# Optimization experiments

Measured on AMD Instinct MI355X. Metric: run time of the kernel, lower is better.

Reference implementation:

```python
import jax, jax.numpy as jnp
import numpy as np

B, T, H, L = 8, 256, 64, 3
NB, NF, HP = 17, 68, 6
K = 9  # temporal kernel
PAD = (K - 1) // 2
EPS = 1e-5


def _normalize(adj):
    adj = adj + np.eye(adj.shape[0], dtype=np.float32)
    d = adj.sum(1)
    dinv = np.power(d, -0.5)
    dinv[np.isinf(dinv)] = 0.0
    return (dinv[:, None] * adj * dinv[None, :]).astype(np.float32)


def _body_adj():
    a = np.zeros((NB, NB), np.float32)
    conns = [(0, 1), (0, 2), (1, 3), (2, 4), (0, 5), (0, 6), (5, 6), (5, 7), (7, 9), (6, 8), (8, 10), (5, 11), (6, 12), (11, 12), (11, 13), (13, 15), (12, 14), (14, 16)]
    for i, j in conns:
        a[i, j] = 1.0
        a[j, i] = 1.0
    return _normalize(a)


def _face_adj():
    a = np.zeros((NF, NF), np.float32)
    for i in range(16): a[i, i + 1] = 1.0
    for i in range(17, 21): a[i, i + 1] = 1.0
    for i in range(22, 26): a[i, i + 1] = 1.0
    for i in range(27, 30): a[i, i + 1] = 1.0
    for i in range(31, 35): a[i, i + 1] = 1.0
    for i in range(36, 41): a[i, i + 1] = 1.0
    a[41, 36] = 1.0
    for i in range(42, 47): a[i, i + 1] = 1.0
    a[47, 42] = 1.0
    for i in range(48, 59): a[i, i + 1] = 1.0
    a[59, 48] = 1.0
    for i in range(60, 67): a[i, i + 1] = 1.0
    a[67, 60] = 1.0
    a = a + a.T
    return _normalize(a)


def setup_inputs() -> dict:
    keys = iter(jax.random.split(jax.random.key(0), 80))

    def rn(shape, s):
        return jax.random.normal(next(keys), shape, jnp.float32) * s

    inp = {}
    inp['body_kps'] = jax.random.normal(next(keys), (B, T, NB * 2), jnp.float32)
    inp['face_kps_2d'] = jax.random.normal(next(keys), (B, T, NF * 2), jnp.float32)
    inp['head_pose'] = jax.random.normal(next(keys), (B, T, HP), jnp.float32)
    inp['body_adj'] = jnp.asarray(_body_adj())
    inp['face_adj'] = jnp.asarray(_face_adj())
    inp['body_proj_w'] = rn((2, H), 0.5)
    inp['body_proj_b'] = jnp.zeros((H,), jnp.float32)
    inp['face_proj_w'] = rn((2, H), 0.5)
    inp['face_proj_b'] = jnp.zeros((H,), jnp.float32)
    inp['head_w'] = rn((HP, H), 0.3)
    inp['head_b'] = jnp.zeros((H,), jnp.float32)
    for p in ('b', 'f'):
        inp[p + '_t1w'] = rn((L, H, H, K), 0.04)
        inp[p + '_t1b'] = jnp.zeros((L, H), jnp.float32)
        inp[p + '_bn1g'] = jnp.ones((L, H), jnp.float32)
        inp[p + '_bn1b'] = jnp.zeros((L, H), jnp.float32)
        inp[p + '_bn1m'] = rn((L, H), 0.1)
        inp[p + '_bn1v'] = jax.random.uniform(next(keys), (L, H), jnp.float32, 0.5, 1.5)
        inp[p + '_gcw'] = rn((L, H, H), 0.1)
        inp[p + '_gcb'] = jnp.zeros((L, H), jnp.float32)
        inp[p + '_t2w'] = rn((L, H, H, K), 0.04)
        inp[p + '_t2b'] = jnp.zeros((L, H), jnp.float32)
        inp[p + '_bn2g'] = jnp.ones((L, H), jnp.float32)
        inp[p + '_bn2b'] = jnp.zeros((L, H), jnp.float32)
        inp[p + '_bn2m'] = rn((L, H), 0.1)
        inp[p + '_bn2v'] = jax.random.uniform(next(keys), (L, H), jnp.float32, 0.5, 1.5)
    total = NB * H + NF * H + H  # 5504
    inp['fus1_w'] = rn((total, 4 * H), 0.02)
    inp['fus1_b'] = jnp.zeros((4 * H,), jnp.float32)
    inp['fus2_w'] = rn((4 * H, 2 * H), 0.06)
    inp['fus2_b'] = jnp.zeros((2 * H,), jnp.float32)
    inp['fus3_w'] = rn((2 * H, H), 0.09)
    inp['fus3_b'] = jnp.zeros((H,), jnp.float32)
    inp['fus4_w'] = rn((H, 5), 0.12)
    inp['fus4_b'] = jnp.zeros((5,), jnp.float32)
    return inp


def _conv_bn(x, w, b, g, be, m, v):
    # x: (BN, C, T); w: (O, I, K). Conv1d (pad=4) + eval-mode BatchNorm1d.
    y = jax.lax.conv_general_dilated(x, w, (1,), [(PAD, PAD)], dimension_numbers=('NCH', 'OIH', 'NCH'))
    y = y + b[None, :, None]
    inv = g * jax.lax.rsqrt(v + EPS)
    return y * inv[None, :, None] + (be - m * inv)[None, :, None]


def _block(x, adj, t1w, t1b, g1, b1, m1, v1, gw, gb, t2w, t2b, g2, b2, m2, v2):
    # x: (B, N, C, T); residual is identity (in_channels == out_channels)
    Bn, N, C, Tn = x.shape
    res = x
    h = jax.nn.relu(_conv_bn(x.reshape(Bn * N, C, Tn), t1w, t1b, g1, b1, m1, v1)).reshape(Bn, N, C, Tn)
    # spatial graph conv, batched over all timesteps at once (adj @ (x W) + b)
    support = jnp.einsum('bnct,co->bnot', h, gw)
    h = jax.nn.relu(jnp.einsum('mn,bnot->bmot', adj, support) + gb[None, None, :, None])
    h = _conv_bn(h.reshape(Bn * N, C, Tn), t2w, t2b, g2, b2, m2, v2).reshape(Bn, N, C, Tn)
    return h + res  # dropout = identity in eval


def _stream(x, n_nodes, pw, pb, adj, ps):
    Bn, Tn, _ = x.shape
    h = x.reshape(Bn, Tn, n_nodes, 2) @ pw + pb          # (B, T, N, H)
    h = jnp.transpose(h, (0, 2, 3, 1))                   # (B, N, H, T)
    for l in range(ps[0].shape[0]):
        h = _block(h, adj, *(p[l] for p in ps))
    return h.mean(axis=3).reshape(Bn, -1)                # temporal mean-pool, flatten nodes


def reference(body_kps, face_kps_2d, head_pose, body_adj, face_adj, body_proj_w, body_proj_b, face_proj_w, face_proj_b, head_w, head_b, b_t1w, b_t1b, b_bn1g, b_bn1b, b_bn1m, b_bn1v, b_gcw, b_gcb, b_t2w, b_t2b, b_bn2g, b_bn2b, b_bn2m, b_bn2v, f_t1w, f_t1b, f_bn1g, f_bn1b, f_bn1m, f_bn1v, f_gcw, f_gcb, f_t2w, f_t2b, f_bn2g, f_bn2b, f_bn2m, f_bn2v, fus1_w, fus1_b, fus2_w, fus2_b, fus3_w, fus3_b, fus4_w, fus4_b):
    bps = (b_t1w, b_t1b, b_bn1g, b_bn1b, b_bn1m, b_bn1v, b_gcw, b_gcb, b_t2w, b_t2b, b_bn2g, b_bn2b, b_bn2m, b_bn2v)
    fps = (f_t1w, f_t1b, f_bn1g, f_bn1b, f_bn1m, f_bn1v, f_gcw, f_gcb, f_t2w, f_t2b, f_bn2g, f_bn2b, f_bn2m, f_bn2v)
    bf = _stream(body_kps, NB, body_proj_w, body_proj_b, body_adj, bps)
    ff = _stream(face_kps_2d, NF, face_proj_w, face_proj_b, face_adj, fps)
    hp = jax.nn.relu(head_pose @ head_w + head_b).mean(axis=1)
    feat = jnp.concatenate([bf, ff, hp], axis=-1)
    h = jax.nn.relu(feat @ fus1_w + fus1_b)
    h = jax.nn.relu(h @ fus2_w + fus2_b)
    h = jax.nn.relu(h @ fus3_w + fus3_b)
    return h @ fus4_w + fus4_b
```

## Files before the change

kernel.cpp:

```cpp
#include <hip/hip_runtime.h>

constexpr int B_ = 8, T_ = 256, H_ = 64, L_ = 3, NB_ = 17, NF_ = 68, HP_ = 6, K_ = 9;
constexpr int FEAT_DIM = NB_ * H_ + NF_ * H_ + H_;
constexpr int HT = H_ * T_;

typedef _Float16 half4_t __attribute__((ext_vector_type(4)));
typedef _Float16 half8_t __attribute__((ext_vector_type(8)));
typedef float f32x16 __attribute__((ext_vector_type(16)));
typedef float f32x4 __attribute__((ext_vector_type(4)));

constexpr size_t SZ_AB = (size_t)B_ * NB_ * HT;
constexpr size_t SZ_AF = (size_t)B_ * NF_ * HT;
constexpr size_t OFF_AB   = 0;
constexpr size_t OFF_AF   = OFF_AB + SZ_AB;
constexpr size_t OFF_SUPB = OFF_AF + SZ_AF;
constexpr size_t OFF_SUPF = OFF_SUPB + SZ_AB / 2;
constexpr size_t OFF_GB   = OFF_SUPF + SZ_AF / 2;
constexpr size_t OFF_GF   = OFF_GB + SZ_AB / 2;
constexpr size_t OFF_W3   = OFF_GF + SZ_AF / 2;
constexpr size_t OFF_GW3  = OFF_W3 + 4 * 55296;
constexpr size_t OFF_B2   = OFF_GW3 + 2 * 6144;
constexpr size_t OFF_ADJPB= OFF_B2 + 768;
constexpr size_t OFF_ADJPF= OFF_ADJPB + 512;
constexpr size_t OFF_FEAT = OFF_ADJPF + 3840;
constexpr size_t OFF_P1   = OFF_FEAT + (size_t)B_ * FEAT_DIM;

struct ConvPrepSet { const float *w, *tb, *g, *bb, *m, *v; };

__global__ __launch_bounds__(256) void prep_convW_all(ConvPrepSet s0, ConvPrepSet s1,
                                                      ConvPrepSet s2, ConvPrepSet s3,
                                                      _Float16* __restrict__ w3,
                                                      float* __restrict__ b2) {
    int set = blockIdx.y;
    ConvPrepSet s = (set == 0) ? s0 : (set == 1) ? s1 : (set == 2) ? s2 : s3;
    int idx = blockIdx.x * 256 + threadIdx.x;
    int k = idx % K_; int r = idx / K_;
    int i = r % H_; r /= H_;
    int o = r % H_; int l = r / H_;
    float sc = s.g[l * H_ + o] * rsqrtf(s.v[l * H_ + o] + 1e-5f);
    w3[(size_t)set * 110592 + ((((l * K_ + k) * 8 + (i >> 3)) * H_ + o) * 8) + (i & 7)]
        = (_Float16)(s.w[idx] * sc);
    if (i == 0 && k == 0)
        b2[set * 192 + l * H_ + o] =
            s.tb[l * H_ + o] * sc + s.bb[l * H_ + o] - s.m[l * H_ + o] * sc;
}

__global__ __launch_bounds__(256) void prep_gcw_all(const float* __restrict__ g0,
                                                    const float* __restrict__ g1,
                                                    _Float16* __restrict__ w3) {
    int set = blockIdx.y;
    const float* gw = set ? g1 : g0;
    int idx = blockIdx.x * 256 + threadIdx.x;
    int o = idx % H_; int r = idx / H_;
    int c = r % H_; int l = r / H_;
    w3[(size_t)set * 12288 + (((l * 8 + (c >> 3)) * H_ + o) * 8) + (c & 7)] = (_Float16)gw[idx];
}

__global__ __launch_bounds__(256) void prep_misc(const float* __restrict__ adjB,
                                                 const float* __restrict__ adjF,
                                                 _Float16* __restrict__ pB,
                                                 _Float16* __restrict__ pF,
                                                 float* __restrict__ p1) {
    int idx = blockIdx.x * 256 + threadIdx.x;
    if (idx < 32 * 32) {
        int m = idx >> 5, k = idx & 31;
        pB[idx] = (m < NB_ && k < NB_) ? (_Float16)adjB[m * NB_ + k] : (_Float16)0.f;
    } else if (idx < 1024 + 96 * 80) {
        int j = idx - 1024;
        int m = j / 80, k = j % 80;
        pF[j] = (m < NF_ && k < NF_) ? (_Float16)adjF[m * NF_ + k] : (_Float16)0.f;
    } else if (idx < 1024 + 7680 + B_ * 256) {
        p1[idx - 8704] = 0.f;
    }
}

__global__ __launch_bounds__(256) void proj_kernel(const float* __restrict__ kpsB,
                                                   const float* __restrict__ pwB,
                                                   const float* __restrict__ pbB,
                                                   float* __restrict__ outB,
                                                   const float* __restrict__ kpsF,
                                                   const float* __restrict__ pwF,
                                                   const float* __restrict__ pbF,
                                                   float* __restrict__ outF,
                                                   int nblk0) {
    int blk = blockIdx.x;
    const float *kps, *pw, *pb; float* out; int N, bn;
    if (blk < nblk0) { kps = kpsB; pw = pwB; pb = pbB; out = outB; N = NB_; bn = blk; }
    else { kps = kpsF; pw = pwF; pb = pbF; out = outF; N = NF_; bn = blk - nblk0; }
    int b = bn / N, n = bn % N;
    int t = threadIdx.x;
    float x0 = kps[((size_t)b * T_ + t) * (N * 2) + n * 2 + 0];
    float x1 = kps[((size_t)b * T_ + t) * (N * 2) + n * 2 + 1];
    float* ob = out + (size_t)bn * HT + t;
#pragma unroll 8
    for (int c = 0; c < H_; ++c)
        ob[(size_t)c * T_] = fmaf(x0, pw[c], fmaf(x1, pw[H_ + c], pb[c]));
}

__device__ __forceinline__ half8_t ld_b8(const _Float16* p) {
    half4_t lo = *(const half4_t*)p;
    half4_t hi = *(const half4_t*)(p + 4);
    return __builtin_shufflevector(lo, hi, 0, 1, 2, 3, 4, 5, 6, 7);
}

__global__ __launch_bounds__(256) void convmix_kernel(
        const float* __restrict__ x0, const half8_t* __restrict__ w30,
        const float* __restrict__ b20, const half8_t* __restrict__ gw0,
        _Float16* __restrict__ sup0,
        const float* __restrict__ x1, const half8_t* __restrict__ w31,
        const float* __restrict__ b21, const half8_t* __restrict__ gw1,
        _Float16* __restrict__ sup1,
        int nblk0, int l) {
    __shared__ __align__(16) _Float16 Xs[136 * 68];
    int blk = blockIdx.x;
    const float* xp; const half8_t* w3; const float* b2v; const half8_t* gwv; _Float16* sup;
    if (blk < nblk0) { xp = x0; w3 = w30; b2v = b20; gwv = gw0; sup = sup0; }
    else { blk -= nblk0; xp = x1; w3 = w31; b2v = b21; gwv = gw1; sup = sup1; }
    int bn = blk >> 1, tc = blk & 1;
    int tid = threadIdx.x;
    const float* xb = xp + (size_t)bn * HT;

    for (int u = tid; u < H_ * 17; u += 256) {
        int c = u / 17, s = u % 17;
        int t0 = tc * 128 + s * 8 - 4;
        const float* xr = xb + (size_t)c * T_;
        _Float16 v[8];
        if (t0 >= 0 && t0 + 8 <= T_) {
            f32x4 a = *(const f32x4*)(xr + t0);
            f32x4 bq = *(const f32x4*)(xr + t0 + 4);
#pragma unroll
            for (int j = 0; j < 4; ++j) { v[j] = (_Float16)a[j]; v[4 + j] = (_Float16)bq[j]; }
        } else {
#pragma unroll
            for (int j = 0; j < 8; ++j) {
                int t = t0 + j;
                v[j] = (t >= 0 && t < T_) ? (_Float16)xr[t] : (_Float16)0.f;
            }
        }
        int tt = s * 8;
#pragma unroll
        for (int j = 0; j < 8; ++j) Xs[(tt + j) * 68 + c] = v[j];
    }
    __syncthreads();

    int ln = tid & 63;
    int w = __builtin_amdgcn_readfirstlane(tid >> 6);
    int ln31 = ln & 31, kg = ln >> 5;

    f32x16 acc[2];
#pragma unroll
    for (int mt = 0; mt < 2; ++mt)
#pragma unroll
        for (int r = 0; r < 16; ++r) acc[mt][r] = 0.f;

    const half8_t* wl = w3 + (size_t)l * (K_ * 8 * H_);
    const _Float16* xrow0 = Xs + (size_t)(w * 32 + ln31) * 68;
#pragma unroll
    for (int tap = 0; tap < K_; ++tap) {
#pragma unroll
        for (int ks = 0; ks < 4; ++ks) {
            int i8 = ks * 2 + kg;
            half8_t a0 = wl[(tap * 8 + i8) * H_ + ln31];
            half8_t a1 = wl[(tap * 8 + i8) * H_ + 32 + ln31];
            half8_t bf = ld_b8(xrow0 + tap * 68 + i8 * 8);
            acc[0] = __builtin_amdgcn_mfma_f32_32x32x16_f16(a0, bf, acc[0], 0, 0, 0);
            acc[1] = __builtin_amdgcn_mfma_f32_32x32x16_f16(a1, bf, acc[1], 0, 0, 0);
        }
    }
    __syncthreads();

    {
        _Float16* mrow = Xs + (size_t)(4 + w * 32 + ln31) * 68;
#pragma unroll
        for (int mt = 0; mt < 2; ++mt) {
#pragma unroll
            for (int rg = 0; rg < 4; ++rg) {
                int o0 = mt * 32 + rg * 8 + kg * 4;
                f32x4 bv = *(const f32x4*)(b2v + l * H_ + o0);
                half4_t hv;
#pragma unroll
                for (int j = 0; j < 4; ++j)
                    hv[j] = (_Float16)fmaxf(acc[mt][rg * 4 + j] + bv[j], 0.f);
                *(half4_t*)(mrow + o0) = hv;
            }
        }
    }
    __syncthreads();

    f32x16 acc2[2];
#pragma unroll
    for (int mt = 0; mt < 2; ++mt)
#pragma unroll
        for (int r = 0; r < 16; ++r) acc2[mt][r] = 0.f;

    const half8_t* gl = gwv + (size_t)l * (8 * H_);
    const _Float16* mrow = Xs + (size_t)(4 + w * 32 + ln31) * 68;
#pragma unroll
    for (int ks = 0; ks < 4; ++ks) {
        int i8 = ks * 2 + kg;
        half8_t a0 = gl[i8 * H_ + ln31];
        half8_t a1 = gl[i8 * H_ + 32 + ln31];
        half8_t bf = ld_b8(mrow + i8 * 8);
        acc2[0] = __builtin_amdgcn_mfma_f32_32x32x16_f16(a0, bf, acc2[0], 0, 0, 0);
        acc2[1] = __builtin_amdgcn_mfma_f32_32x32x16_f16(a1, bf, acc2[1], 0, 0, 0);
    }

    int t = tc * 128 + w * 32 + ln31;
    _Float16* sp = sup + (size_t)bn * HT + t;
#pragma unroll
    for (int mt = 0; mt < 2; ++mt) {
#pragma unroll
        for (int r = 0; r < 16; ++r) {
            int o = mt * 32 + (r & 3) + 8 * (r >> 2) + 4 * kg;
            sp[(size_t)o * T_] = (_Float16)acc2[mt][r];
        }
    }
}

__global__ __launch_bounds__(256) void conv2_kernel(
        const _Float16* __restrict__ x0, const half8_t* __restrict__ w30,
        const float* __restrict__ b20, float* __restrict__ trunk0,
        const _Float16* __restrict__ x1, const half8_t* __restrict__ w31,
        const float* __restrict__ b21, float* __restrict__ trunk1,
        int nblk0, int l) {
    __shared__ __align__(16) _Float16 Xs[136 * 68];
    int blk = blockIdx.x;
    const _Float16* xp; const half8_t* w3; const float* b2v; float* trunk;
    if (blk < nblk0) { xp = x0; w3 = w30; b2v = b20; trunk = trunk0; }
    else { blk -= nblk0; xp = x1; w3 = w31; b2v = b21; trunk = trunk1; }
    int bn = blk >> 1, tc = blk & 1;
    int tid = threadIdx.x;
    const _Float16* xb = xp + (size_t)bn * HT;

    for (int u = tid; u < H_ * 17; u += 256) {
        int c = u / 17, s = u % 17;
        int t0 = tc * 128 + s * 8 - 4;
        const _Float16* xr = xb + (size_t)c * T_;
        _Float16 v[8];
        if (t0 >= 0 && t0 + 8 <= T_) {
            half4_t a = *(const half4_t*)(xr + t0);
            half4_t bq = *(const half4_t*)(xr + t0 + 4);
#pragma unroll
            for (int j = 0; j < 4; ++j) { v[j] = a[j]; v[4 + j] = bq[j]; }
        } else {
#pragma unroll
            for (int j = 0; j < 8; ++j) {
                int t = t0 + j;
                v[j] = (t >= 0 && t < T_) ? xr[t] : (_Float16)0.f;
            }
        }
        int tt = s * 8;
#pragma unroll
        for (int j = 0; j < 8; ++j) Xs[(tt + j) * 68 + c] = v[j];
    }
    __syncthreads();

    int ln = tid & 63;
    int w = __builtin_amdgcn_readfirstlane(tid >> 6);
    int ln31 = ln & 31, kg = ln >> 5;

    f32x16 acc[2];
#pragma unroll
    for (int mt = 0; mt < 2; ++mt)
#pragma unroll
        for (int r = 0; r < 16; ++r) acc[mt][r] = 0.f;

    const half8_t* wl = w3 + (size_t)l * (K_ * 8 * H_);
    const _Float16* xrow0 = Xs + (size_t)(w * 32 + ln31) * 68;
#pragma unroll
    for (int tap = 0; tap < K_; ++tap) {
#pragma unroll
        for (int ks = 0; ks < 4; ++ks) {
            int i8 = ks * 2 + kg;
            half8_t a0 = wl[(tap * 8 + i8) * H_ + ln31];
            half8_t a1 = wl[(tap * 8 + i8) * H_ + 32 + ln31];
            half8_t bf = ld_b8(xrow0 + tap * 68 + i8 * 8);
            acc[0] = __builtin_amdgcn_mfma_f32_32x32x16_f16(a0, bf, acc[0], 0, 0, 0);
            acc[1] = __builtin_amdgcn_mfma_f32_32x32x16_f16(a1, bf, acc[1], 0, 0, 0);
        }
    }

    int t = tc * 128 + w * 32 + ln31;
    float* tp = trunk + (size_t)bn * HT + t;
#pragma unroll
    for (int mt = 0; mt < 2; ++mt) {
#pragma unroll
        for (int r = 0; r < 16; ++r) {
            int o = mt * 32 + (r & 3) + 8 * (r >> 2) + 4 * kg;
            float bias = b2v[l * H_ + o];
            tp[(size_t)o * T_] += acc[mt][r] + bias;
        }
    }
}

template <int N, int MT, int KS>
__device__ __forceinline__ void adjmix_impl(const _Float16* __restrict__ sup,
                                            const half8_t* __restrict__ adjP,
                                            const float* __restrict__ gb,
                                            _Float16* __restrict__ out,
                                            int blk, int l, _Float16* Ls, int tid) {
    constexpr int KP = KS * 16;
    constexpr int PITCH = KP + 4;
    int b = blk >> 7, cb = blk & 127;
    int colbase = cb * 128;
    float gbv = gb[l * H_ + (cb >> 1)];

    for (int u = tid; u < KP * 16; u += 256) {
        int n = u >> 4, cs = u & 15;
        half8_t v;
        if (n < N) v = *(const half8_t*)(sup + (size_t)(b * N + n) * HT + colbase + cs * 8);
        else {
#pragma unroll
            for (int j = 0; j < 8; ++j) v[j] = (_Float16)0.f;
        }
#pragma unroll
        for (int j = 0; j < 8; ++j) Ls[(cs * 8 + j) * PITCH + n] = v[j];
    }
    __syncthreads();

    int ln = tid & 63;
    int w = __builtin_amdgcn_readfirstlane(tid >> 6);
    int ln31 = ln & 31, kg = ln >> 5;
    int colL = w * 32 + ln31;

    f32x16 acc[MT];
#pragma unroll
    for (int mt = 0; mt < MT; ++mt)
#pragma unroll
        for (int r = 0; r < 16; ++r) acc[mt][r] = 0.f;

#pragma unroll
    for (int ks = 0; ks < KS; ++ks) {
        half8_t bf = ld_b8(&Ls[colL * PITCH + ks * 16 + kg * 8]);
#pragma unroll
        for (int mt = 0; mt < MT; ++mt) {
            half8_t af = adjP[(size_t)(mt * 32 + ln31) * (KP / 8) + ks * 2 + kg];
            acc[mt] = __builtin_amdgcn_mfma_f32_32x32x16_f16(af, bf, acc[mt], 0, 0, 0);
        }
    }

    int col = colbase + colL;
#pragma unroll
    for (int mt = 0; mt < MT; ++mt) {
#pragma unroll
        for (int r = 0; r < 16; ++r) {
            int m = mt * 32 + (r & 3) + 8 * (r >> 2) + 4 * kg;
            if (m < N)
                out[(size_t)(b * N + m) * HT + col] = (_Float16)fmaxf(acc[mt][r] + gbv, 0.f);
        }
    }
}

__global__ __launch_bounds__(256) void adjmix_kernel(
        const _Float16* __restrict__ supB, const half8_t* __restrict__ adjPB,
        const float* __restrict__ gbB, _Float16* __restrict__ outB,
        const _Float16* __restrict__ supF, const half8_t* __restrict__ adjPF,
        const float* __restrict__ gbF, _Float16* __restrict__ outF,
        int nblk0, int l) {
    __shared__ __align__(16) _Float16 Ls[128 * 84];
    int blk = blockIdx.x, tid = threadIdx.x;
    if (blk < nblk0)
        adjmix_impl<NB_, 1, 2>(supB, adjPB, gbB, outB, blk, l, Ls, tid);
    else
        adjmix_impl<NF_, 3, 5>(supF, adjPF, gbF, outF, blk - nblk0, l, Ls, tid);
}

__global__ __launch_bounds__(256) void meanpool_kernel(const float* __restrict__ xB,
                                                       const float* __restrict__ xF,
                                                       float* __restrict__ feat, int nblk0) {
    __shared__ float red[256];
    int blk = blockIdx.x;
    const float* x; int N, bn, base;
    if (blk < nblk0) { x = xB; N = NB_; bn = blk; base = 0; }
    else { x = xF; N = NF_; bn = blk - nblk0; base = NB_ * H_; }
    int b = bn / N, n = bn % N;
    int tid = threadIdx.x;
    int c = tid >> 2, q = tid & 3;
    const float* xb = x + ((size_t)bn * H_ + c) * T_;
    float acc = 0.f;
#pragma unroll 8
    for (int j = 0; j < 64; ++j) acc += xb[q + 4 * j];
    red[tid] = acc;
    __syncthreads();
    if (q == 0) {
        float s = red[tid] + red[tid + 1] + red[tid + 2] + red[tid + 3];
        feat[(size_t)b * FEAT_DIM + base + n * H_ + c] = s * (1.f / 256.f);
    }
}

__global__ void head_kernel(const float* __restrict__ x, const float* __restrict__ hw,
                            const float* __restrict__ hb, float* __restrict__ feat) {
    int b = blockIdx.x;
    int c = threadIdx.x;
    float w0 = hw[c], w1 = hw[64 + c], w2 = hw[128 + c],
          w3 = hw[192 + c], w4 = hw[256 + c], w5 = hw[320 + c];
    float bias = hb[c];
    float acc = 0.f;
    for (int t = 0; t < T_; ++t) {
        const float* xr = x + ((size_t)b * T_ + t) * HP_;
        float s = fmaf(xr[0], w0, fmaf(xr[1], w1, fmaf(xr[2], w2,
                  fmaf(xr[3], w3, fmaf(xr[4], w4, fmaf(xr[5], w5, bias))))));
        acc += fmaxf(s, 0.f);
    }
    feat[(size_t)b * FEAT_DIM + NB_ * H_ + NF_ * H_ + c] = acc * (1.f / 256.f);
}

__global__ __launch_bounds__(256) void fus1_kernel(const float* __restrict__ feat,
                                                   const float* __restrict__ w1,
                                                   float* __restrict__ p1) {
    __shared__ float fv[128];
    int b = blockIdx.x / 43, ic = blockIdx.x % 43;
    int tid = threadIdx.x;
    if (tid < 128) fv[tid] = feat[(size_t)b * FEAT_DIM + ic * 128 + tid];
    __syncthreads();
    const float* wb = w1 + (size_t)(ic * 128) * 256 + tid;
    float acc = 0.f;
#pragma unroll 4
    for (int i = 0; i < 128; ++i)
        acc = fmaf(fv[i], wb[(size_t)i * 256], acc);
    atomicAdd(&p1[b * 256 + tid], acc);
}

__global__ __launch_bounds__(256) void fus_tail_kernel(const float* __restrict__ p1,
        const float* __restrict__ b1, const float* __restrict__ w2, const float* __restrict__ b2,
        const float* __restrict__ w3, const float* __restrict__ b3,
        const float* __restrict__ w4, const float* __restrict__ b4, float* __restrict__ out) {
    __shared__ float s1[256], s2[128], s3[64];
    int b = blockIdx.x, tid = threadIdx.x;
    s1[tid] = fmaxf(p1[b * 256 + tid] + b1[tid], 0.f);
    __syncthreads();
    if (tid < 128) {
        float acc = b2[tid];
        for (int i = 0; i < 256; ++i) acc = fmaf(s1[i], w2[i * 128 + tid], acc);
        s2[tid] = fmaxf(acc, 0.f);
    }
    __syncthreads();
    if (tid < 64) {
        float acc = b3[tid];
        for (int i = 0; i < 128; ++i) acc = fmaf(s2[i], w3[i * 64 + tid], acc);
        s3[tid] = fmaxf(acc, 0.f);
    }
    __syncthreads();
    if (tid < 5) {
        float acc = b4[tid];
        for (int i = 0; i < 64; ++i) acc = fmaf(s3[i], w4[i * 5 + tid], acc);
        out[b * 5 + tid] = acc;
    }
}

extern "C" void kernel_launch(void* const* d_in, const int* in_sizes, int n_in,
                              void* d_out, int out_size, void* d_ws, size_t ws_size,
                              hipStream_t stream) {
    const float* body_kps = (const float*)d_in[0];
    const float* face_kps = (const float*)d_in[1];
    const float* head_pose = (const float*)d_in[2];
    const float* body_adj = (const float*)d_in[3];
    const float* face_adj = (const float*)d_in[4];
    const float* body_pw = (const float*)d_in[5];
    const float* body_pb = (const float*)d_in[6];
    const float* face_pw = (const float*)d_in[7];
    const float* face_pb = (const float*)d_in[8];
    const float* head_w = (const float*)d_in[9];
    const float* head_b = (const float*)d_in[10];
    const float* b_t1w = (const float*)d_in[11]; const float* b_t1b = (const float*)d_in[12];
    const float* b_g1  = (const float*)d_in[13]; const float* b_b1  = (const float*)d_in[14];
    const float* b_m1  = (const float*)d_in[15]; const float* b_v1  = (const float*)d_in[16];
    const float* b_gcw = (const float*)d_in[17]; const float* b_gcb = (const float*)d_in[18];
    const float* b_t2w = (const float*)d_in[19]; const float* b_t2b = (const float*)d_in[20];
    const float* b_g2  = (const float*)d_in[21]; const float* b_b2  = (const float*)d_in[22];
    const float* b_m2  = (const float*)d_in[23]; const float* b_v2  = (const float*)d_in[24];
    const float* f_t1w = (const float*)d_in[25]; const float* f_t1b = (const float*)d_in[26];
    const float* f_g1  = (const float*)d_in[27]; const float* f_b1  = (const float*)d_in[28];
    const float* f_m1  = (const float*)d_in[29]; const float* f_v1  = (const float*)d_in[30];
    const float* f_gcw = (const float*)d_in[31]; const float* f_gcb = (const float*)d_in[32];
    const float* f_t2w = (const float*)d_in[33]; const float* f_t2b = (const float*)d_in[34];
    const float* f_g2  = (const float*)d_in[35]; const float* f_b2  = (const float*)d_in[36];
    const float* f_m2  = (const float*)d_in[37]; const float* f_v2  = (const float*)d_in[38];
    const float* fus1_w = (const float*)d_in[39]; const float* fus1_b = (const float*)d_in[40];
    const float* fus2_w = (const float*)d_in[41]; const float* fus2_b = (const float*)d_in[42];
    const float* fus3_w = (const float*)d_in[43]; const float* fus3_b = (const float*)d_in[44];
    const float* fus4_w = (const float*)d_in[45]; const float* fus4_b = (const float*)d_in[46];

    float* ws = (float*)d_ws;
    float* A_body = ws + OFF_AB;
    float* A_face = ws + OFF_AF;
    _Float16* SupB = (_Float16*)(ws + OFF_SUPB);
    _Float16* SupF = (_Float16*)(ws + OFF_SUPF);
    _Float16* Gb = (_Float16*)(ws + OFF_GB);
    _Float16* Gf = (_Float16*)(ws + OFF_GF);
    _Float16* W3 = (_Float16*)(ws + OFF_W3);
    _Float16* W3b1 = W3;            _Float16* W3b2 = W3 + 110592;
    _Float16* W3f1 = W3 + 221184;   _Float16* W3f2 = W3 + 331776;
    _Float16* GW3 = (_Float16*)(ws + OFF_GW3);
    _Float16* GW3b = GW3;           _Float16* GW3f = GW3 + 12288;
    float* B2 = ws + OFF_B2;
    float* B2b1 = B2;        float* B2b2 = B2 + 192;
    float* B2f1 = B2 + 384;  float* B2f2 = B2 + 576;
    _Float16* adjPB = (_Float16*)(ws + OFF_ADJPB);
    _Float16* adjPF = (_Float16*)(ws + OFF_ADJPF);
    float* feat = ws + OFF_FEAT;
    float* p1 = ws + OFF_P1;
    float* out = (float*)d_out;

    ConvPrepSet sb1{b_t1w, b_t1b, b_g1, b_b1, b_m1, b_v1};
    ConvPrepSet sb2{b_t2w, b_t2b, b_g2, b_b2, b_m2, b_v2};
    ConvPrepSet sf1{f_t1w, f_t1b, f_g1, f_b1, f_m1, f_v1};
    ConvPrepSet sf2{f_t2w, f_t2b, f_g2, f_b2, f_m2, f_v2};
    prep_convW_all<<<dim3(432, 4), 256, 0, stream>>>(sb1, sb2, sf1, sf2, W3, B2);
    prep_gcw_all<<<dim3(48, 2), 256, 0, stream>>>(b_gcw, f_gcw, GW3);
    prep_misc<<<42, 256, 0, stream>>>(body_adj, face_adj, adjPB, adjPF, p1);

    const int nB = B_ * NB_;
    const int nF = B_ * NF_;
    proj_kernel<<<nB + nF, 256, 0, stream>>>(body_kps, body_pw, body_pb, A_body,
                                             face_kps, face_pw, face_pb, A_face, nB);

    const int gb = nB * 2;
    const int gf = nF * 2;
    const int ga = B_ * 128;

    for (int l = 0; l < L_; ++l) {
        convmix_kernel<<<gb + gf, 256, 0, stream>>>(
            A_body, (const half8_t*)W3b1, B2b1, (const half8_t*)GW3b, SupB,
            A_face, (const half8_t*)W3f1, B2f1, (const half8_t*)GW3f, SupF, gb, l);
        adjmix_kernel<<<2 * ga, 256, 0, stream>>>(SupB, (const half8_t*)adjPB, b_gcb, Gb,
                                                  SupF, (const half8_t*)adjPF, f_gcb, Gf, ga, l);
        conv2_kernel<<<gb + gf, 256, 0, stream>>>(
            Gb, (const half8_t*)W3b2, B2b2, A_body,
            Gf, (const half8_t*)W3f2, B2f2, A_face, gb, l);
    }

    meanpool_kernel<<<nB + nF, 256, 0, stream>>>(A_body, A_face, feat, nB);
    head_kernel<<<B_, 64, 0, stream>>>(head_pose, head_w, head_b, feat);
    fus1_kernel<<<B_ * 43, 256, 0, stream>>>(feat, fus1_w, p1);
    fus_tail_kernel<<<B_, 256, 0, stream>>>(p1, fus1_b, fus2_w, fus2_b, fus3_w, fus3_b,
                                            fus4_w, fus4_b, out);
}
```

Before: 447.5 us.

## Fuse conv2 with next layer's conv1+gcn mix, fp16 trunk, fold meanpool

Stores the residual trunk in fp16 instead of fp32. Fuses each layer's second temporal conv (with residual) into the next layer's first conv and graph-weight mix, so one block processes a full 256-step sequence. The final layer's conv2 is fused with temporal mean pooling through atomics into a zeroed feature buffer. This removes a kernel launch per layer, the fp32 trunk traffic and the separate meanpool pass. In exchange, the fp16 trunk loses precision, the grid has half as many blocks, and LDS use per block is larger.

```diff
diff --git a/kernel.cpp b/kernel.cpp
--- a/kernel.cpp
+++ b/kernel.cpp
@@ -11,9 +11,9 @@
 
 constexpr size_t SZ_AB = (size_t)B_ * NB_ * HT;
 constexpr size_t SZ_AF = (size_t)B_ * NF_ * HT;
-constexpr size_t OFF_AB   = 0;
-constexpr size_t OFF_AF   = OFF_AB + SZ_AB;
-constexpr size_t OFF_SUPB = OFF_AF + SZ_AF;
+constexpr size_t OFF_TB   = 0;
+constexpr size_t OFF_TF   = OFF_TB + SZ_AB / 2;
+constexpr size_t OFF_SUPB = OFF_TF + SZ_AF / 2;
 constexpr size_t OFF_SUPF = OFF_SUPB + SZ_AB / 2;
 constexpr size_t OFF_GB   = OFF_SUPF + SZ_AF / 2;
 constexpr size_t OFF_GF   = OFF_GB + SZ_AB / 2;
@@ -60,41 +60,44 @@
                                                  const float* __restrict__ adjF,
                                                  _Float16* __restrict__ pB,
                                                  _Float16* __restrict__ pF,
-                                                 float* __restrict__ p1) {
+                                                 float* __restrict__ p1,
+                                                 float* __restrict__ feat) {
     int idx = blockIdx.x * 256 + threadIdx.x;
-    if (idx < 32 * 32) {
+    if (idx < 1024) {
         int m = idx >> 5, k = idx & 31;
         pB[idx] = (m < NB_ && k < NB_) ? (_Float16)adjB[m * NB_ + k] : (_Float16)0.f;
-    } else if (idx < 1024 + 96 * 80) {
+    } else if (idx < 8704) {
         int j = idx - 1024;
         int m = j / 80, k = j % 80;
         pF[j] = (m < NF_ && k < NF_) ? (_Float16)adjF[m * NF_ + k] : (_Float16)0.f;
-    } else if (idx < 1024 + 7680 + B_ * 256) {
+    } else if (idx < 10752) {
         p1[idx - 8704] = 0.f;
+    } else if (idx < 10752 + B_ * FEAT_DIM) {
+        feat[idx - 10752] = 0.f;
     }
 }
 
 __global__ __launch_bounds__(256) void proj_kernel(const float* __restrict__ kpsB,
                                                    const float* __restrict__ pwB,
                                                    const float* __restrict__ pbB,
-                                                   float* __restrict__ outB,
+                                                   _Float16* __restrict__ outB,
                                                    const float* __restrict__ kpsF,
                                                    const float* __restrict__ pwF,
                                                    const float* __restrict__ pbF,
-                                                   float* __restrict__ outF,
+                                                   _Float16* __restrict__ outF,
                                                    int nblk0) {
     int blk = blockIdx.x;
-    const float *kps, *pw, *pb; float* out; int N, bn;
+    const float *kps, *pw, *pb; _Float16* out; int N, bn;
     if (blk < nblk0) { kps = kpsB; pw = pwB; pb = pbB; out = outB; N = NB_; bn = blk; }
     else { kps = kpsF; pw = pwF; pb = pbF; out = outF; N = NF_; bn = blk - nblk0; }
     int b = bn / N, n = bn % N;
     int t = threadIdx.x;
     float x0 = kps[((size_t)b * T_ + t) * (N * 2) + n * 2 + 0];
     float x1 = kps[((size_t)b * T_ + t) * (N * 2) + n * 2 + 1];
-    float* ob = out + (size_t)bn * HT + t;
+    _Float16* ob = out + (size_t)bn * HT + t;
 #pragma unroll 8
     for (int c = 0; c < H_; ++c)
-        ob[(size_t)c * T_] = fmaf(x0, pw[c], fmaf(x1, pw[H_ + c], pb[c]));
+        ob[(size_t)c * T_] = (_Float16)fmaf(x0, pw[c], fmaf(x1, pw[H_ + c], pb[c]));
 }
 
 __device__ __forceinline__ half8_t ld_b8(const _Float16* p) {
@@ -103,138 +106,30 @@
     return __builtin_shufflevector(lo, hi, 0, 1, 2, 3, 4, 5, 6, 7);
 }
 
-__global__ __launch_bounds__(256) void convmix_kernel(
-        const float* __restrict__ x0, const half8_t* __restrict__ w30,
-        const float* __restrict__ b20, const half8_t* __restrict__ gw0,
-        _Float16* __restrict__ sup0,
-        const float* __restrict__ x1, const half8_t* __restrict__ w31,
-        const float* __restrict__ b21, const half8_t* __restrict__ gw1,
-        _Float16* __restrict__ sup1,
-        int nblk0, int l) {
-    __shared__ __align__(16) _Float16 Xs[136 * 68];
+struct StreamP {
+    const _Float16* x;
+    const _Float16* res;
+    _Float16* trunk_out;
+    const half8_t* w2; const float* b2;
+    const half8_t* w1; const float* b1;
+    const half8_t* gc;
+    _Float16* sup;
+    int N; int featbase;
+};
+
+template <int MODE>
+__global__ __launch_bounds__(256) void fused_kernel(StreamP P0, StreamP P1, int nblk0,
+                                                    int l2, int l1, float* __restrict__ feat) {
+    __shared__ __align__(16) _Float16 Xs[264 * 68];
     int blk = blockIdx.x;
-    const float* xp; const half8_t* w3; const float* b2v; const half8_t* gwv; _Float16* sup;
-    if (blk < nblk0) { xp = x0; w3 = w30; b2v = b20; gwv = gw0; sup = sup0; }
-    else { blk -= nblk0; xp = x1; w3 = w31; b2v = b21; gwv = gw1; sup = sup1; }
-    int bn = blk >> 1, tc = blk & 1;
+    StreamP P = (blk < nblk0) ? P0 : P1;
+    int bn = (blk < nblk0) ? blk : blk - nblk0;
     int tid = threadIdx.x;
-    const float* xb = xp + (size_t)bn * HT;
-
-    for (int u = tid; u < H_ * 17; u += 256) {
-        int c = u / 17, s = u % 17;
-        int t0 = tc * 128 + s * 8 - 4;
-        const float* xr = xb + (size_t)c * T_;
-        _Float16 v[8];
-        if (t0 >= 0 && t0 + 8 <= T_) {
-            f32x4 a = *(const f32x4*)(xr + t0);
-            f32x4 bq = *(const f32x4*)(xr + t0 + 4);
-#pragma unroll
-            for (int j = 0; j < 4; ++j) { v[j] = (_Float16)a[j]; v[4 + j] = (_Float16)bq[j]; }
-        } else {
-#pragma unroll
-            for (int j = 0; j < 8; ++j) {
-                int t = t0 + j;
-                v[j] = (t >= 0 && t < T_) ? (_Float16)xr[t] : (_Float16)0.f;
-            }
-        }
-        int tt = s * 8;
-#pragma unroll
-        for (int j = 0; j < 8; ++j) Xs[(tt + j) * 68 + c] = v[j];
-    }
-    __syncthreads();
-
-    int ln = tid & 63;
-    int w = __builtin_amdgcn_readfirstlane(tid >> 6);
-    int ln31 = ln & 31, kg = ln >> 5;
-
-    f32x16 acc[2];
-#pragma unroll
-    for (int mt = 0; mt < 2; ++mt)
-#pragma unroll
-        for (int r = 0; r < 16; ++r) acc[mt][r] = 0.f;
-
-    const half8_t* wl = w3 + (size_t)l * (K_ * 8 * H_);
-    const _Float16* xrow0 = Xs + (size_t)(w * 32 + ln31) * 68;
-#pragma unroll
-    for (int tap = 0; tap < K_; ++tap) {
-#pragma unroll
-        for (int ks = 0; ks < 4; ++ks) {
-            int i8 = ks * 2 + kg;
-            half8_t a0 = wl[(tap * 8 + i8) * H_ + ln31];
-            half8_t a1 = wl[(tap * 8 + i8) * H_ + 32 + ln31];
-            half8_t bf = ld_b8(xrow0 + tap * 68 + i8 * 8);
-            acc[0] = __builtin_amdgcn_mfma_f32_32x32x16_f16(a0, bf, acc[0], 0, 0, 0);
-            acc[1] = __builtin_amdgcn_mfma_f32_32x32x16_f16(a1, bf, acc[1], 0, 0, 0);
-        }
-    }
-    __syncthreads();
-
-    {
-        _Float16* mrow = Xs + (size_t)(4 + w * 32 + ln31) * 68;
-#pragma unroll
-        for (int mt = 0; mt < 2; ++mt) {
-#pragma unroll
-            for (int rg = 0; rg < 4; ++rg) {
-                int o0 = mt * 32 + rg * 8 + kg * 4;
-                f32x4 bv = *(const f32x4*)(b2v + l * H_ + o0);
-                half4_t hv;
-#pragma unroll
-                for (int j = 0; j < 4; ++j)
-                    hv[j] = (_Float16)fmaxf(acc[mt][rg * 4 + j] + bv[j], 0.f);
-                *(half4_t*)(mrow + o0) = hv;
-            }
-        }
-    }
-    __syncthreads();
-
-    f32x16 acc2[2];
-#pragma unroll
-    for (int mt = 0; mt < 2; ++mt)
-#pragma unroll
-        for (int r = 0; r < 16; ++r) acc2[mt][r] = 0.f;
-
-    const half8_t* gl = gwv + (size_t)l * (8 * H_);
-    const _Float16* mrow = Xs + (size_t)(4 + w * 32 + ln31) * 68;
-#pragma unroll
-    for (int ks = 0; ks < 4; ++ks) {
-        int i8 = ks * 2 + kg;
-        half8_t a0 = gl[i8 * H_ + ln31];
-        half8_t a1 = gl[i8 * H_ + 32 + ln31];
-        half8_t bf = ld_b8(mrow + i8 * 8);
-        acc2[0] = __builtin_amdgcn_mfma_f32_32x32x16_f16(a0, bf, acc2[0], 0, 0, 0);
-        acc2[1] = __builtin_amdgcn_mfma_f32_32x32x16_f16(a1, bf, acc2[1], 0, 0, 0);
-    }
-
-    int t = tc * 128 + w * 32 + ln31;
-    _Float16* sp = sup + (size_t)bn * HT + t;
-#pragma unroll
-    for (int mt = 0; mt < 2; ++mt) {
-#pragma unroll
-        for (int r = 0; r < 16; ++r) {
-            int o = mt * 32 + (r & 3) + 8 * (r >> 2) + 4 * kg;
-            sp[(size_t)o * T_] = (_Float16)acc2[mt][r];
-        }
-    }
-}
-
-__global__ __launch_bounds__(256) void conv2_kernel(
-        const _Float16* __restrict__ x0, const half8_t* __restrict__ w30,
-        const float* __restrict__ b20, float* __restrict__ trunk0,
-        const _Float16* __restrict__ x1, const half8_t* __restrict__ w31,
-        const float* __restrict__ b21, float* __restrict__ trunk1,
-        int nblk0, int l) {
-    __shared__ __align__(16) _Float16 Xs[136 * 68];
-    int blk = blockIdx.x;
-    const _Float16* xp; const half8_t* w3; const float* b2v; float* trunk;
-    if (blk < nblk0) { xp = x0; w3 = w30; b2v = b20; trunk = trunk0; }
-    else { blk -= nblk0; xp = x1; w3 = w31; b2v = b21; trunk = trunk1; }
-    int bn = blk >> 1, tc = blk & 1;
-    int tid = threadIdx.x;
-    const _Float16* xb = xp + (size_t)bn * HT;
-
-    for (int u = tid; u < H_ * 17; u += 256) {
-        int c = u / 17, s = u % 17;
-        int t0 = tc * 128 + s * 8 - 4;
+
+    const _Float16* xb = P.x + (size_t)bn * HT;
+    for (int u = tid; u < 64 * 33; u += 256) {
+        int c = u / 33, s = u % 33;
+        int t0 = s * 8 - 4;
         const _Float16* xr = xb + (size_t)c * T_;
         _Float16 v[8];
         if (t0 >= 0 && t0 + 8 <= T_) {
@@ -249,46 +144,175 @@
                 v[j] = (t >= 0 && t < T_) ? xr[t] : (_Float16)0.f;
             }
         }
-        int tt = s * 8;
-#pragma unroll
-        for (int j = 0; j < 8; ++j) Xs[(tt + j) * 68 + c] = v[j];
+        int row = s * 8;
+#pragma unroll
+        for (int j = 0; j < 8; ++j) Xs[(row + j) * 68 + c] = v[j];
     }
     __syncthreads();
 
     int ln = tid & 63;
     int w = __builtin_amdgcn_readfirstlane(tid >> 6);
     int ln31 = ln & 31, kg = ln >> 5;
-
-    f32x16 acc[2];
+    int tb0 = w * 64;
+
+    if (MODE >= 1) {
+        f32x16 c2[2][2];
+#pragma unroll
+        for (int mt = 0; mt < 2; ++mt)
+#pragma unroll
+            for (int ts = 0; ts < 2; ++ts)
+#pragma unroll
+                for (int r = 0; r < 16; ++r) c2[mt][ts][r] = 0.f;
+        const half8_t* wl = P.w2 + (size_t)l2 * (K_ * 8 * H_);
+#pragma unroll
+        for (int tap = 0; tap < K_; ++tap) {
+#pragma unroll
+            for (int ks = 0; ks < 4; ++ks) {
+                int i8 = ks * 2 + kg;
+                half8_t a0 = wl[(tap * 8 + i8) * H_ + ln31];
+                half8_t a1 = wl[(tap * 8 + i8) * H_ + 32 + ln31];
+#pragma unroll
+                for (int ts = 0; ts < 2; ++ts) {
+                    half8_t bf = ld_b8(&Xs[(tb0 + ts * 32 + ln31 + tap) * 68 + i8 * 8]);
+                    c2[0][ts] = __builtin_amdgcn_mfma_f32_32x32x16_f16(a0, bf, c2[0][ts], 0, 0, 0);
+                    c2[1][ts] = __builtin_amdgcn_mfma_f32_32x32x16_f16(a1, bf, c2[1][ts], 0, 0, 0);
+                }
+            }
+        }
+        __syncthreads();
+
+        const _Float16* resb = P.res + (size_t)bn * HT;
+        if (MODE == 1) {
+            _Float16* tob = P.trunk_out + (size_t)bn * HT;
+#pragma unroll
+            for (int mt = 0; mt < 2; ++mt) {
+#pragma unroll
+                for (int ts = 0; ts < 2; ++ts) {
+                    int t = tb0 + ts * 32 + ln31;
+#pragma unroll
+                    for (int r = 0; r < 16; ++r) {
+                        int o = mt * 32 + (r & 3) + 8 * (r >> 2) + 4 * kg;
+                        float mv = c2[mt][ts][r] + P.b2[l2 * H_ + o]
+                                 + (float)resb[(size_t)o * T_ + t];
+                        _Float16 h = (_Float16)mv;
+                        Xs[(t + 4) * 68 + o] = h;
+                        tob[(size_t)o * T_ + t] = h;
+                    }
+                }
+            }
+            __syncthreads();
+        } else {
+            float* red = (float*)Xs;
+            float sv[2][16];
+#pragma unroll
+            for (int mt = 0; mt < 2; ++mt) {
+#pragma unroll
+                for (int r = 0; r < 16; ++r) {
+                    int o = mt * 32 + (r & 3) + 8 * (r >> 2) + 4 * kg;
+                    float bias = P.b2[l2 * H_ + o];
+                    float s = c2[mt][0][r] + bias + (float)resb[(size_t)o * T_ + tb0 + ln31]
+                            + c2[mt][1][r] + bias + (float)resb[(size_t)o * T_ + tb0 + 32 + ln31];
+#pragma unroll
+                    for (int m = 1; m < 32; m <<= 1) s += __shfl_xor(s, m, 64);
+                    sv[mt][r] = s;
+                }
+            }
+            if (ln31 == 0) {
+#pragma unroll
+                for (int mt = 0; mt < 2; ++mt)
+#pragma unroll
+                    for (int r = 0; r < 16; ++r) {
+                        int o = mt * 32 + (r & 3) + 8 * (r >> 2) + 4 * kg;
+                        red[w * 64 + o] = sv[mt][r];
+                    }
+            }
+            __syncthreads();
+            if (tid < 64) {
+                float s = red[tid] + red[64 + tid] + red[128 + tid] + red[192 + tid];
+                int b = bn / P.N, n = bn % P.N;
+                atomicAdd(&feat[(size_t)b * FEAT_DIM + P.featbase + n * H_ + tid],
+                          s * (1.f / 256.f));
+            }
+            return;
+        }
+    }
+
+    f32x16 a1c[2][2];
 #pragma unroll
     for (int mt = 0; mt < 2; ++mt)
 #pragma unroll
-        for (int r = 0; r < 16; ++r) acc[mt][r] = 0.f;
-
-    const half8_t* wl = w3 + (size_t)l * (K_ * 8 * H_);
-    const _Float16* xrow0 = Xs + (size_t)(w * 32 + ln31) * 68;
+        for (int ts = 0; ts < 2; ++ts)
+#pragma unroll
+            for (int r = 0; r < 16; ++r) a1c[mt][ts][r] = 0.f;
+    const half8_t* wl1 = P.w1 + (size_t)l1 * (K_ * 8 * H_);
 #pragma unroll
     for (int tap = 0; tap < K_; ++tap) {
 #pragma unroll
         for (int ks = 0; ks < 4; ++ks) {
             int i8 = ks * 2 + kg;
-            half8_t a0 = wl[(tap * 8 + i8) * H_ + ln31];
-            half8_t a1 = wl[(tap * 8 + i8) * H_ + 32 + ln31];
-            half8_t bf = ld_b8(xrow0 + tap * 68 + i8 * 8);
-            acc[0] = __builtin_amdgcn_mfma_f32_32x32x16_f16(a0, bf, acc[0], 0, 0, 0);
-            acc[1] = __builtin_amdgcn_mfma_f32_32x32x16_f16(a1, bf, acc[1], 0, 0, 0);
-        }
-    }
-
-    int t = tc * 128 + w * 32 + ln31;
-    float* tp = trunk + (size_t)bn * HT + t;
+            half8_t a0 = wl1[(tap * 8 + i8) * H_ + ln31];
+            half8_t a1 = wl1[(tap * 8 + i8) * H_ + 32 + ln31];
+#pragma unroll
+            for (int ts = 0; ts < 2; ++ts) {
+                half8_t bf = ld_b8(&Xs[(tb0 + ts * 32 + ln31 + tap) * 68 + i8 * 8]);
+                a1c[0][ts] = __builtin_amdgcn_mfma_f32_32x32x16_f16(a0, bf, a1c[0][ts], 0, 0, 0);
+                a1c[1][ts] = __builtin_amdgcn_mfma_f32_32x32x16_f16(a1, bf, a1c[1][ts], 0, 0, 0);
+            }
+        }
+    }
+    __syncthreads();
+
 #pragma unroll
     for (int mt = 0; mt < 2; ++mt) {
 #pragma unroll
-        for (int r = 0; r < 16; ++r) {
-            int o = mt * 32 + (r & 3) + 8 * (r >> 2) + 4 * kg;
-            float bias = b2v[l * H_ + o];
-            tp[(size_t)o * T_] += acc[mt][r] + bias;
+        for (int rg = 0; rg < 4; ++rg) {
+            int o0 = mt * 32 + rg * 8 + kg * 4;
+            f32x4 bv = *(const f32x4*)(P.b1 + l1 * H_ + o0);
+#pragma unroll
+            for (int ts = 0; ts < 2; ++ts) {
+                int t = tb0 + ts * 32 + ln31;
+                half4_t hv;
+#pragma unroll
+                for (int j = 0; j < 4; ++j)
+                    hv[j] = (_Float16)fmaxf(a1c[mt][ts][rg * 4 + j] + bv[j], 0.f);
+                *(half4_t*)(&Xs[(t + 4) * 68 + o0]) = hv;
+            }
+        }
+    }
+    __syncthreads();
+
+    f32x16 m2[2][2];
+#pragma unroll
+    for (int mt = 0; mt < 2; ++mt)
+#pragma unroll
+        for (int ts = 0; ts < 2; ++ts)
+#pragma unroll
+            for (int r = 0; r < 16; ++r) m2[mt][ts][r] = 0.f;
+    const half8_t* gl = P.gc + (size_t)l1 * (8 * H_);
+#pragma unroll
+    for (int ks = 0; ks < 4; ++ks) {
+        int i8 = ks * 2 + kg;
+        half8_t a0 = gl[i8 * H_ + ln31];
+        half8_t a1 = gl[i8 * H_ + 32 + ln31];
+#pragma unroll
+        for (int ts = 0; ts < 2; ++ts) {
+            half8_t bf = ld_b8(&Xs[(tb0 + ts * 32 + ln31 + 4) * 68 + i8 * 8]);
+            m2[0][ts] = __builtin_amdgcn_mfma_f32_32x32x16_f16(a0, bf, m2[0][ts], 0, 0, 0);
+            m2[1][ts] = __builtin_amdgcn_mfma_f32_32x32x16_f16(a1, bf, m2[1][ts], 0, 0, 0);
+        }
+    }
+
+    _Float16* sp = P.sup + (size_t)bn * HT;
+#pragma unroll
+    for (int mt = 0; mt < 2; ++mt) {
+#pragma unroll
+        for (int ts = 0; ts < 2; ++ts) {
+            int t = tb0 + ts * 32 + ln31;
+#pragma unroll
+            for (int r = 0; r < 16; ++r) {
+                int o = mt * 32 + (r & 3) + 8 * (r >> 2) + 4 * kg;
+                sp[(size_t)o * T_ + t] = (_Float16)m2[mt][ts][r];
+            }
         }
     }
 }
@@ -363,29 +387,6 @@
         adjmix_impl<NB_, 1, 2>(supB, adjPB, gbB, outB, blk, l, Ls, tid);
     else
         adjmix_impl<NF_, 3, 5>(supF, adjPF, gbF, outF, blk - nblk0, l, Ls, tid);
-}
-
-__global__ __launch_bounds__(256) void meanpool_kernel(const float* __restrict__ xB,
-                                                       const float* __restrict__ xF,
-                                                       float* __restrict__ feat, int nblk0) {
-    __shared__ float red[256];
-    int blk = blockIdx.x;
-    const float* x; int N, bn, base;
-    if (blk < nblk0) { x = xB; N = NB_; bn = blk; base = 0; }
-    else { x = xF; N = NF_; bn = blk - nblk0; base = NB_ * H_; }
-    int b = bn / N, n = bn % N;
-    int tid = threadIdx.x;
-    int c = tid >> 2, q = tid & 3;
-    const float* xb = x + ((size_t)bn * H_ + c) * T_;
-    float acc = 0.f;
-#pragma unroll 8
-    for (int j = 0; j < 64; ++j) acc += xb[q + 4 * j];
-    red[tid] = acc;
-    __syncthreads();
-    if (q == 0) {
-        float s = red[tid] + red[tid + 1] + red[tid + 2] + red[tid + 3];
-        feat[(size_t)b * FEAT_DIM + base + n * H_ + c] = s * (1.f / 256.f);
-    }
 }
 
 __global__ void head_kernel(const float* __restrict__ x, const float* __restrict__ hw,
@@ -482,8 +483,8 @@
     const float* fus4_w = (const float*)d_in[45]; const float* fus4_b = (const float*)d_in[46];
 
     float* ws = (float*)d_ws;
-    float* A_body = ws + OFF_AB;
-    float* A_face = ws + OFF_AF;
+    _Float16* TrB = (_Float16*)(ws + OFF_TB);
+    _Float16* TrF = (_Float16*)(ws + OFF_TF);
     _Float16* SupB = (_Float16*)(ws + OFF_SUPB);
     _Float16* SupF = (_Float16*)(ws + OFF_SUPF);
     _Float16* Gb = (_Float16*)(ws + OFF_GB);
@@ -508,29 +509,33 @@
     ConvPrepSet sf2{f_t2w, f_t2b, f_g2, f_b2, f_m2, f_v2};
     prep_convW_all<<<dim3(432, 4), 256, 0, stream>>>(sb1, sb2, sf1, sf2, W3, B2);
     prep_gcw_all<<<dim3(48, 2), 256, 0, stream>>>(b_gcw, f_gcw, GW3);
-    prep_misc<<<42, 256, 0, stream>>>(body_adj, face_adj, adjPB, adjPF, p1);
+    prep_misc<<<214, 256, 0, stream>>>(body_adj, face_adj, adjPB, adjPF, p1, feat);
 
     const int nB = B_ * NB_;
     const int nF = B_ * NF_;
-    proj_kernel<<<nB + nF, 256, 0, stream>>>(body_kps, body_pw, body_pb, A_body,
-                                             face_kps, face_pw, face_pb, A_face, nB);
-
-    const int gb = nB * 2;
-    const int gf = nF * 2;
+    proj_kernel<<<nB + nF, 256, 0, stream>>>(body_kps, body_pw, body_pb, TrB,
+                                             face_kps, face_pw, face_pb, TrF, nB);
+
+    StreamP pb_{TrB, TrB, TrB, (const half8_t*)W3b2, B2b2,
+                (const half8_t*)W3b1, B2b1, (const half8_t*)GW3b, SupB, NB_, 0};
+    StreamP pf_{TrF, TrF, TrF, (const half8_t*)W3f2, B2f2,
+                (const half8_t*)W3f1, B2f1, (const half8_t*)GW3f, SupF, NF_, NB_ * H_};
+    StreamP gb_ = pb_; gb_.x = Gb;
+    StreamP gf_ = pf_; gf_.x = Gf;
+
     const int ga = B_ * 128;
 
-    for (int l = 0; l < L_; ++l) {
-        convmix_kernel<<<gb + gf, 256, 0, stream>>>(
-            A_body, (const half8_t*)W3b1, B2b1, (const half8_t*)GW3b, SupB,
-            A_face, (const half8_t*)W3f1, B2f1, (const half8_t*)GW3f, SupF, gb, l);
-        adjmix_kernel<<<2 * ga, 256, 0, stream>>>(SupB, (const half8_t*)adjPB, b_gcb, Gb,
-                                                  SupF, (const half8_t*)adjPF, f_gcb, Gf, ga, l);
-        conv2_kernel<<<gb + gf, 256, 0, stream>>>(
-            Gb, (const half8_t*)W3b2, B2b2, A_body,
-            Gf, (const half8_t*)W3f2, B2f2, A_face, gb, l);
-    }
-
-    meanpool_kernel<<<nB + nF, 256, 0, stream>>>(A_body, A_face, feat, nB);
+    fused_kernel<0><<<nB + nF, 256, 0, stream>>>(pb_, pf_, nB, 0, 0, feat);
+    adjmix_kernel<<<2 * ga, 256, 0, stream>>>(SupB, (const half8_t*)adjPB, b_gcb, Gb,
+                                              SupF, (const half8_t*)adjPF, f_gcb, Gf, ga, 0);
+    fused_kernel<1><<<nB + nF, 256, 0, stream>>>(gb_, gf_, nB, 0, 1, feat);
+    adjmix_kernel<<<2 * ga, 256, 0, stream>>>(SupB, (const half8_t*)adjPB, b_gcb, Gb,
+                                              SupF, (const half8_t*)adjPF, f_gcb, Gf, ga, 1);
+    fused_kernel<1><<<nB + nF, 256, 0, stream>>>(gb_, gf_, nB, 1, 2, feat);
+    adjmix_kernel<<<2 * ga, 256, 0, stream>>>(SupB, (const half8_t*)adjPB, b_gcb, Gb,
+                                              SupF, (const half8_t*)adjPF, f_gcb, Gf, ga, 2);
+    fused_kernel<2><<<nB + nF, 256, 0, stream>>>(gb_, gf_, nB, 2, 2, feat);
+
     head_kernel<<<B_, 64, 0, stream>>>(head_pose, head_w, head_b, feat);
     fus1_kernel<<<B_ * 43, 256, 0, stream>>>(feat, fus1_w, p1);
     fus_tail_kernel<<<B_, 256, 0, stream>>>(p1, fus1_b, fus2_w, fus2_b, fus3_w, fus3_b,
```

After: 475.3 us. +6.2%, slower.
